# Optimization experiments

Measured on AMD Instinct MI355X. Metric: run time of the kernel, lower is better.

Reference implementation:

```python
import jax, jax.numpy as jnp
import numpy as np

N = 30000       # mesh nodes
E = 150000      # mesh edges
L = 128         # latent_size
STEPS = 5       # message_passing_steps
TW = 5          # time_window
TD = 2          # target_dim
NODE_IN = TD + 1 + 9   # u + load + node_type one-hot = 12
EDGE_IN = 2 + 1 + TD   # rel_mesh + dist + grad_u = 5


def _mlp(x, W1, b1, W2, b2, g, be):
    # Linear -> ReLU -> Linear -> ReLU -> LayerNorm (matches MLP module)
    h = jax.nn.relu(x @ W1 + b1)
    h = jax.nn.relu(h @ W2 + b2)
    mu = jnp.mean(h, axis=-1, keepdims=True)
    var = jnp.mean(jnp.square(h - mu), axis=-1, keepdims=True)
    return g * (h - mu) / jnp.sqrt(var + 1e-5) + be


def setup_inputs() -> dict:
    key = jax.random.key(0)
    ks = iter(jax.random.split(key, 64))
    def nrm(shape, s=0.05):
        return jax.random.normal(next(ks), shape, dtype=jnp.float32) * s
    inp = {}
    inp['mesh_pos'] = jax.random.normal(next(ks), (1, N, 2), dtype=jnp.float32)
    inp['node_type'] = jax.random.normal(next(ks), (1, N, 9), dtype=jnp.float32)
    inp['u'] = jax.random.normal(next(ks), (1, N, TD), dtype=jnp.float32)
    inp['load'] = jax.random.normal(next(ks), (1, N, 1), dtype=jnp.float32)
    inp['senders'] = jax.random.randint(next(ks), (E,), 0, N, dtype=jnp.int32)
    inp['receivers'] = jax.random.randint(next(ks), (E,), 0, N, dtype=jnp.int32)
    # node encoder MLP(12 -> 128)
    inp['enc_node_W1'] = nrm((NODE_IN, L)); inp['enc_node_b1'] = nrm((L,), 0.01)
    inp['enc_node_W2'] = nrm((L, L));       inp['enc_node_b2'] = nrm((L,), 0.01)
    inp['enc_node_g'] = jnp.ones((L,), jnp.float32); inp['enc_node_be'] = jnp.zeros((L,), jnp.float32)
    # edge encoder MLP(5 -> 128)
    inp['enc_edge_W1'] = nrm((EDGE_IN, L)); inp['enc_edge_b1'] = nrm((L,), 0.01)
    inp['enc_edge_W2'] = nrm((L, L));       inp['enc_edge_b2'] = nrm((L,), 0.01)
    inp['enc_edge_g'] = jnp.ones((L,), jnp.float32); inp['enc_edge_be'] = jnp.zeros((L,), jnp.float32)
    # STEPS GraphNetBlocks, params stacked along leading axis for lax.scan
    inp['blk_edge_W1'] = nrm((STEPS, 3 * L, L)); inp['blk_edge_b1'] = nrm((STEPS, L), 0.01)
    inp['blk_edge_W2'] = nrm((STEPS, L, L));     inp['blk_edge_b2'] = nrm((STEPS, L), 0.01)
    inp['blk_edge_g'] = jnp.ones((STEPS, L), jnp.float32); inp['blk_edge_be'] = jnp.zeros((STEPS, L), jnp.float32)
    inp['blk_node_W1'] = nrm((STEPS, 2 * L, L)); inp['blk_node_b1'] = nrm((STEPS, L), 0.01)
    inp['blk_node_W2'] = nrm((STEPS, L, L));     inp['blk_node_b2'] = nrm((STEPS, L), 0.01)
    inp['blk_node_g'] = jnp.ones((STEPS, L), jnp.float32); inp['blk_node_be'] = jnp.zeros((STEPS, L), jnp.float32)
    # decoder: Conv1d(L,8,1) -> Swish -> Conv1d(8, TD*TW, 1); kernel-size-1 conv == per-node linear
    inp['dec_W1'] = nrm((L, 8)); inp['dec_b1'] = nrm((8,), 0.01)
    inp['dec_W2'] = nrm((8, TD * TW)); inp['dec_b2'] = nrm((TD * TW,), 0.01)
    return inp


def reference(mesh_pos, node_type, u, load, senders, receivers,
              enc_node_W1, enc_node_b1, enc_node_W2, enc_node_b2, enc_node_g, enc_node_be,
              enc_edge_W1, enc_edge_b1, enc_edge_W2, enc_edge_b2, enc_edge_g, enc_edge_be,
              blk_edge_W1, blk_edge_b1, blk_edge_W2, blk_edge_b2, blk_edge_g, blk_edge_be,
              blk_node_W1, blk_node_b1, blk_node_W2, blk_node_b2, blk_node_g, blk_node_be,
              dec_W1, dec_b1, dec_W2, dec_b2):
    # --- encode ---
    node_feats = jnp.concatenate([u, load, node_type], axis=-1)        # [1,N,12]
    nl = _mlp(node_feats, enc_node_W1, enc_node_b1, enc_node_W2, enc_node_b2, enc_node_g, enc_node_be)
    rel = mesh_pos[:, senders] - mesh_pos[:, receivers]                # [1,E,2]
    dist = jnp.linalg.norm(rel, axis=-1, keepdims=True)                # [1,E,1]
    grad_u = u[:, senders] - u[:, receivers]                           # [1,E,2]
    ef = jnp.concatenate([rel, dist, grad_u], axis=-1)                 # [1,E,5]
    el = _mlp(ef, enc_edge_W1, enc_edge_b1, enc_edge_W2, enc_edge_b2, enc_edge_g, enc_edge_be)
    n_nodes = nl.shape[1]

    # --- process: GraphNetBlocks with residual connections ---
    def block(carry, p):
        nl, el = carry
        edge_in = jnp.concatenate([nl[:, senders], nl[:, receivers], el], axis=-1)  # [1,E,3L]
        ne = _mlp(edge_in, p['eW1'], p['eb1'], p['eW2'], p['eb2'], p['eg'], p['ebe'])
        aggr = jax.vmap(lambda e: jax.ops.segment_sum(e, receivers, num_segments=n_nodes))(ne)  # [1,N,L]
        node_in = jnp.concatenate([nl, aggr], axis=-1)                 # [1,N,2L]
        nn = _mlp(node_in, p['nW1'], p['nb1'], p['nW2'], p['nb2'], p['ng'], p['nbe'])
        return (nl + nn, el + ne), None

    ps = {'eW1': blk_edge_W1, 'eb1': blk_edge_b1, 'eW2': blk_edge_W2, 'eb2': blk_edge_b2,
          'eg': blk_edge_g, 'ebe': blk_edge_be,
          'nW1': blk_node_W1, 'nb1': blk_node_b1, 'nW2': blk_node_W2, 'nb2': blk_node_b2,
          'ng': blk_node_g, 'nbe': blk_node_be}
    (nl, el), _ = jax.lax.scan(block, (nl, el), ps)

    # --- decode (1x1 Conv1d == per-node linear) ---
    h = nl @ dec_W1 + dec_b1
    h = h * jax.nn.sigmoid(h)                                          # Swish(beta=1)
    decoded = h @ dec_W2 + dec_b2                                      # [1,N,TW*TD]
    dt = jnp.repeat(jnp.arange(1, TW + 1, dtype=decoded.dtype), TD)    # [TW*TD]
    delta = (decoded * dt).reshape(-1, TW, TD).transpose(1, 0, 2)      # [TW,N,TD]
    return delta
```

## Files before the change

### kernel.cpp

```cpp
#include <hip/hip_runtime.h>
#include <hip/hip_bf16.h>

#define LNUM 128
#define NNODES 30000
#define NEDGES 150000
#define NSTEPS 5


typedef _Float16 f16;
typedef __attribute__((ext_vector_type(2))) _Float16 f16x2;
typedef __attribute__((ext_vector_type(8))) _Float16 f16x8;
typedef __attribute__((ext_vector_type(4))) float f32x4;

__device__ __forceinline__ void glds16(const void* g, void* l) {
    __builtin_amdgcn_global_load_lds(
        (const __attribute__((address_space(1))) void*)g,
        (__attribute__((address_space(3))) void*)l, 16, 0, 0);
}

__device__ __forceinline__ void atomic_pk_add(f16* addr, f16 lo, f16 hi) {
#if __has_builtin(__builtin_amdgcn_global_atomic_fadd_v2f16)
    f16x2 v; v[0] = lo; v[1] = hi;
    __builtin_amdgcn_global_atomic_fadd_v2f16(
        (__attribute__((address_space(1))) f16x2*)addr, v);
#else
    uint32_t* p = (uint32_t*)addr;
    uint32_t old = *p, assumed;
    do {
        assumed = old;
        union { uint32_t u; f16 h[2]; } c; c.u = assumed;
        c.h[0] += lo; c.h[1] += hi;
        old = atomicCAS(p, assumed, c.u);
    } while (old != assumed);
#endif
}

template<int ROWS, int K, int KP>
__device__ __forceinline__ void mlp_apply(
    const float* __restrict__ xs, float* __restrict__ hv,
    float* __restrict__ mu_s, float* __restrict__ rs_s,
    const float* __restrict__ W1, const float* __restrict__ b1,
    const float* __restrict__ W2, const float* __restrict__ b2,
    const float* __restrict__ g,  const float* __restrict__ be,
    float out[ROWS])
{
    const int t = threadIdx.x;
    float acc[ROWS];
    {
        const float bb = b1[t];
        #pragma unroll
        for (int r = 0; r < ROWS; r++) acc[r] = bb;
    }
    int k = 0;
    for (; k + 4 <= K; k += 4) {
        const float w0 = W1[(k + 0) * LNUM + t];
        const float w1 = W1[(k + 1) * LNUM + t];
        const float w2 = W1[(k + 2) * LNUM + t];
        const float w3 = W1[(k + 3) * LNUM + t];
        #pragma unroll
        for (int r = 0; r < ROWS; r++) {
            const float4 x = *(const float4*)(xs + r * KP + k);
            acc[r] = fmaf(x.x, w0, acc[r]);
            acc[r] = fmaf(x.y, w1, acc[r]);
            acc[r] = fmaf(x.z, w2, acc[r]);
            acc[r] = fmaf(x.w, w3, acc[r]);
        }
    }
    for (; k < K; ++k) {
        const float w = W1[k * LNUM + t];
        #pragma unroll
        for (int r = 0; r < ROWS; r++) acc[r] = fmaf(xs[r * KP + k], w, acc[r]);
    }
    #pragma unroll
    for (int r = 0; r < ROWS; r++) hv[r * LNUM + t] = fmaxf(acc[r], 0.f);
    __syncthreads();
    {
        const float bb = b2[t];
        #pragma unroll
        for (int r = 0; r < ROWS; r++) acc[r] = bb;
    }
    for (int k2 = 0; k2 < LNUM; k2 += 4) {
        const float w0 = W2[(k2 + 0) * LNUM + t];
        const float w1 = W2[(k2 + 1) * LNUM + t];
        const float w2 = W2[(k2 + 2) * LNUM + t];
        const float w3 = W2[(k2 + 3) * LNUM + t];
        #pragma unroll
        for (int r = 0; r < ROWS; r++) {
            const float4 x = *(const float4*)(hv + r * LNUM + k2);
            acc[r] = fmaf(x.x, w0, acc[r]);
            acc[r] = fmaf(x.y, w1, acc[r]);
            acc[r] = fmaf(x.z, w2, acc[r]);
            acc[r] = fmaf(x.w, w3, acc[r]);
        }
    }
    __syncthreads();
    #pragma unroll
    for (int r = 0; r < ROWS; r++) hv[r * LNUM + t] = fmaxf(acc[r], 0.f);
    __syncthreads();
    if (t < ROWS) {
        float s = 0.f, s2 = 0.f;
        for (int kk = 0; kk < LNUM; kk++) {
            const float v = hv[t * LNUM + kk];
            s += v; s2 += v * v;
        }
        const float m = s * (1.0f / LNUM);
        mu_s[t] = m;
        rs_s[t] = rsqrtf(fmaxf(s2 * (1.0f / LNUM) - m * m, 0.f) + 1e-5f);
    }
    __syncthreads();
    const float gg = g[t], bbe = be[t];
    #pragma unroll
    for (int r = 0; r < ROWS; r++)
        out[r] = fmaf(gg * (hv[r * LNUM + t] - mu_s[r]), rs_s[r], bbe);
}

__global__ __launch_bounds__(128) void encode_nodes_k(
    const float* __restrict__ u, const float* __restrict__ load_,
    const float* __restrict__ ntype,
    const float* __restrict__ W1, const float* __restrict__ b1,
    const float* __restrict__ W2, const float* __restrict__ b2,
    const float* __restrict__ g,  const float* __restrict__ be,
    f16* __restrict__ nl)
{
    constexpr int ROWS = 4, K = 12, KP = 12;
    __shared__ __align__(16) float xs[ROWS * KP];
    __shared__ __align__(16) float hv[ROWS * LNUM];
    __shared__ float mu_s[ROWS], rs_s[ROWS];
    const int t = threadIdx.x;
    const int base = blockIdx.x * ROWS;
    if (t < ROWS * K) {
        const int r = t / K, k = t % K;
        const int n = base + r;
        float v;
        if (k < 2)      v = u[n * 2 + k];
        else if (k < 3) v = load_[n];
        else            v = ntype[n * 9 + (k - 3)];
        xs[r * KP + k] = v;
    }
    __syncthreads();
    float out[ROWS];
    mlp_apply<ROWS, K, KP>(xs, hv, mu_s, rs_s, W1, b1, W2, b2, g, be, out);
    #pragma unroll
    for (int r = 0; r < ROWS; r++) nl[(base + r) * LNUM + t] = (f16)out[r];
}

#define PE1 245760
#define PE2 81920
#define PN1 163840
#define PN2 81920
#define PQ1 4096
#define PQ2 16384
#define PTOT (PE1+PE2+PN1+PN2+PQ1+PQ2)

__global__ __launch_bounds__(256) void prep_w_all_k(
    const float* __restrict__ eW1, const float* __restrict__ eW2,
    const float* __restrict__ nW1, const float* __restrict__ nW2,
    const float* __restrict__ qW1, const float* __restrict__ qW2,
    f16* __restrict__ out)
{
    int j = blockIdx.x * 256 + threadIdx.x;
    if (j >= PTOT) return;
    const float* W; int K, kreal; f16* hi; f16* p = out;
    if (j < PE1) { W = eW1; K = 384; kreal = 384; hi = p; }
    else { p += PE1; j -= PE1;
    if (j < PE2) { W = eW2; K = 128; kreal = 128; hi = p; }
    else { p += PE2; j -= PE2;
    if (j < PN1) { W = nW1; K = 256; kreal = 256; hi = p; }
    else { p += PN1; j -= PN1;
    if (j < PN2) { W = nW2; K = 128; kreal = 128; hi = p; }
    else { p += PN2; j -= PN2;
    if (j < PQ1) { W = qW1; K = 32;  kreal = 5;   hi = p; }
    else { p += PQ1; j -= PQ1;
         { W = qW2; K = 128; kreal = 128; hi = p; } } } } } }
    const int k = j % K;
    const int rem = j / K;
    const int n = rem & 127;
    const int s = rem >> 7;
    const float v = (k < kreal) ? W[((size_t)s * kreal + k) * 128 + n] : 0.f;
    hi[j] = (f16)v;
}

template<int MODE, int NCH1, int K1S>
__global__ __launch_bounds__(256, 5) void mfma_mlp_k(
    const f16* __restrict__ Lat, const float* __restrict__ Fa,
    const float* __restrict__ Fb,
    f16* __restrict__ io, f16* __restrict__ aggr,
    const int* __restrict__ senders, const int* __restrict__ receivers,
    const f16* __restrict__ W1h, const float* __restrict__ b1,
    const f16* __restrict__ W2h, const float* __restrict__ b2,
    const float* __restrict__ gam, const float* __restrict__ bet,
    int nrows)
{
    __shared__ __align__(16) f16 WH[2][4096];
    __shared__ __align__(16) unsigned short Yh[64 * 128];

    const int t  = threadIdx.x;
    const int w  = t >> 6;
    const int l  = t & 63;
    const int lr = l & 15;
    const int lg = l >> 4;
    const int swz = lg ^ ((lr >> 1) & 3);
    const int base = blockIdx.x * 64;

    const int eg  = base + w * 16 + lr;
    const int egc = min(eg, nrows - 1);

    int sv = 0, rv = 0;
    if constexpr (MODE != 1) { sv = senders[egc]; rv = receivers[egc]; }

    float feat[8];
    if constexpr (MODE == 2) {
        const float ax = Fa[sv * 2], ay = Fa[sv * 2 + 1];
        const float bx = Fa[rv * 2], by = Fa[rv * 2 + 1];
        const float rx = ax - bx, ry = ay - by;
        feat[0] = rx; feat[1] = ry; feat[2] = sqrtf(rx * rx + ry * ry);
        feat[3] = Fb[sv * 2] - Fb[rv * 2];
        feat[4] = Fb[sv * 2 + 1] - Fb[rv * 2 + 1];
        feat[5] = 0.f; feat[6] = 0.f; feat[7] = 0.f;
    }

    auto stage = [&](const f16* __restrict__ Wh, const int kst, const int kc,
                     const int buf) {
        #pragma unroll
        for (int i = 0; i < 2; i++) {
            const int c = 2 * w + i;
            const int ophys = c * 1024 + l * 16;
            const int olog  = ophys ^ (((ophys >> 7) & 3) << 4);
            const int row   = olog >> 6;
            const int slot  = (olog >> 4) & 3;
            glds16(Wh + (size_t)row * kst + kc * 32 + slot * 8,
                   (char*)&WH[buf][0] + c * 1024);
        }
    };

    uint4 qnA, qnB, qnC;
    auto prefetchTo = [&](int kc, uint4& q) {
        if constexpr (MODE == 0) {
            const f16* src;
            if (kc < 4)      src = Lat + (size_t)sv  * 128 + kc * 32 + lg * 8;
            else if (kc < 8) src = Lat + (size_t)rv  * 128 + (kc - 4) * 32 + lg * 8;
            else             src = io  + (size_t)egc * 128 + (kc - 8) * 32 + lg * 8;
            q = *(const uint4*)src;
        } else if constexpr (MODE == 1) {
            const f16* src;
            if (kc < 4) src = io  + (size_t)egc * 128 + kc * 32 + lg * 8;
            else        src = Lat + (size_t)egc * 128 + (kc - 4) * 32 + lg * 8;
            q = *(const uint4*)src;
        }
    };

    const f32x4 zero4 = {0.f, 0.f, 0.f, 0.f};
    f32x4 acc[8];
    #pragma unroll
    for (int mf = 0; mf < 8; mf++) acc[mf] = zero4;

    if constexpr (MODE != 2) {
        prefetchTo(0, qnA);
        if constexpr (NCH1 > 1) prefetchTo(1, qnB);
    }
    stage(W1h, K1S, 0, 0);

    #pragma unroll
    for (int kc = 0; kc < NCH1; ++kc) {
        if (MODE != 2 && kc >= 1 && kc + 1 < NCH1)
            asm volatile("s_waitcnt vmcnt(1)" ::: "memory");
        else
            asm volatile("s_waitcnt vmcnt(0)" ::: "memory");
        __builtin_amdgcn_sched_barrier(0);
        __builtin_amdgcn_s_barrier();
        __builtin_amdgcn_sched_barrier(0);
        if (kc + 1 < NCH1) stage(W1h, K1S, kc + 1, (kc + 1) & 1);
        else               stage(W2h, 128,  0,      NCH1 & 1);
        if constexpr (MODE != 2) {
            if (kc + 2 < NCH1) {
                if      ((kc + 2) % 3 == 0) prefetchTo(kc + 2, qnA);
                else if ((kc + 2) % 3 == 1) prefetchTo(kc + 2, qnB);
                else                        prefetchTo(kc + 2, qnC);
            }
        }
        f16x8 XHv, XLv;
        bool useXL = false;
        if constexpr (MODE == 2) {
            union { f16 h[8]; f16x8 v; } uh, ul;
            #pragma unroll
            for (int j = 0; j < 8; j++) {
                const float x = (lg == 0) ? feat[j] : 0.f;
                const f16 h = (f16)x;
                uh.h[j] = h;
                ul.h[j] = (f16)(x - (float)h);
            }
            XHv = uh.v; XLv = ul.v; useXL = true;
        } else {
            union { uint4 q; f16x8 v; } cc;
            cc.q = (kc % 3 == 0) ? qnA : ((kc % 3 == 1) ? qnB : qnC);
            XHv = cc.v;
        }
        #pragma unroll
        for (int mf = 0; mf < 8; mf++) {
            const int off = (mf * 16 + lr) * 64 + (swz << 4);
            const f16x8 wh = *(const f16x8*)((const char*)&WH[kc & 1][0] + off);
            acc[mf] = __builtin_amdgcn_mfma_f32_16x16x32_f16(XHv, wh, acc[mf], 0, 0, 0);
            if (useXL)
                acc[mf] = __builtin_amdgcn_mfma_f32_16x16x32_f16(XLv, wh, acc[mf], 0, 0, 0);
        }
    }

    #pragma unroll
    for (int mf = 0; mf < 8; mf++) {
        const float bb1 = b1[mf * 16 + lr];
        #pragma unroll
        for (int reg = 0; reg < 4; reg++) {
            float v = acc[mf][reg] + bb1;
            v = fmaxf(v, 0.f);
            union { f16 h; unsigned short u; } cc; cc.h = (f16)v;
            const int row = w * 16 + lg * 4 + reg;
            const int cb  = (mf * 16 + lr) * 2;
            *(unsigned short*)((char*)Yh + row * 256 +
                               (cb ^ (((lg * 4 + reg) & 7) << 4))) = cc.u;
        }
        acc[mf] = zero4;
    }

    #pragma unroll
    for (int kc = 0; kc < 4; ++kc) {
        asm volatile("s_waitcnt vmcnt(0)" ::: "memory");
        __builtin_amdgcn_sched_barrier(0);
        __builtin_amdgcn_s_barrier();
        __builtin_amdgcn_sched_barrier(0);
        if (kc + 1 < 4) stage(W2h, 128, kc + 1, (NCH1 + kc + 1) & 1);
        union { uint4 q; f16x8 v; } YH;
        {
            const int row = w * 16 + lr;
            const int cb  = (kc * 32 + lg * 8) * 2;
            YH.q = *(const uint4*)((const char*)Yh + row * 256 +
                                   (cb ^ ((lr & 7) << 4)));
        }
        #pragma unroll
        for (int mf = 0; mf < 8; mf++) {
            const int off = (mf * 16 + lr) * 64 + (swz << 4);
            const f16x8 wh = *(const f16x8*)((const char*)&WH[(NCH1 + kc) & 1][0] + off);
            acc[mf] = __builtin_amdgcn_mfma_f32_16x16x32_f16(YH.v, wh, acc[mf], 0, 0, 0);
        }
    }

    float vv[8][4];
    float s1[4] = {0, 0, 0, 0}, s2[4] = {0, 0, 0, 0};
    #pragma unroll
    for (int mf = 0; mf < 8; mf++) {
        const float bb2 = b2[mf * 16 + lr];
        #pragma unroll
        for (int reg = 0; reg < 4; reg++) {
            float v = acc[mf][reg] + bb2;
            v = fmaxf(v, 0.f);
            vv[mf][reg] = v;
            s1[reg] += v; s2[reg] += v * v;
        }
    }
    #pragma unroll
    for (int m = 1; m < 16; m <<= 1) {
        #pragma unroll
        for (int reg = 0; reg < 4; reg++) {
            s1[reg] += __shfl_xor(s1[reg], m);
            s2[reg] += __shfl_xor(s2[reg], m);
        }
    }
    float gg[8], b8[8];
    #pragma unroll
    for (int mf = 0; mf < 8; mf++) {
        gg[mf] = gam[mf * 16 + lr];
        b8[mf] = bet[mf * 16 + lr];
    }

    #pragma unroll
    for (int reg = 0; reg < 4; reg++) {
        const float mu = s1[reg] * (1.f / 128.f);
        const float rs = rsqrtf(fmaxf(s2[reg] * (1.f / 128.f) - mu * mu, 0.f) + 1e-5f);
        const int row = w * 16 + lg * 4 + reg;
        const int idx = base + row;
        if (idx < nrows) {
            if constexpr (MODE == 0) {
                const int rc = receivers[idx];
                #pragma unroll
                for (int mf = 0; mf < 8; mf++) {
                    const int col = mf * 16 + lr;
                    const float o = gg[mf] * (vv[mf][reg] - mu) * rs + b8[mf];
                    const float op = __shfl_xor(o, 1);
                    if ((lr & 1) == 0)
                        atomic_pk_add(aggr + (size_t)rc * 128 + col,
                                      (f16)o, (f16)op);
                    f16* p = io + (size_t)idx * 128 + col;
                    *p = (f16)((float)*p + o);
                }
            } else if constexpr (MODE == 1) {
                #pragma unroll
                for (int mf = 0; mf < 8; mf++) {
                    const int col = mf * 16 + lr;
                    const float o = gg[mf] * (vv[mf][reg] - mu) * rs + b8[mf];
                    f16* p = io + (size_t)idx * 128 + col;
                    *p = (f16)((float)*p + o);
                }
            } else {
                #pragma unroll
                for (int mf = 0; mf < 8; mf++) {
                    const int col = mf * 16 + lr;
                    const float o = gg[mf] * (vv[mf][reg] - mu) * rs + b8[mf];
                    io[(size_t)idx * 128 + col] = (f16)o;
                }
            }
        }
    }

    if constexpr (MODE == 1) {
        const uint4 z = {0, 0, 0, 0};
        #pragma unroll
        for (int c = 0; c < 4; c++)
            *(uint4*)(aggr + (size_t)egc * 128 + c * 32 + lg * 8) = z;
    }
}

__global__ __launch_bounds__(128) void decode_k(
    const f16* __restrict__ nl,
    const float* __restrict__ W1, const float* __restrict__ b1,
    const float* __restrict__ W2, const float* __restrict__ b2,
    float* __restrict__ out)
{
    constexpr int NPB = 16;
    __shared__ __align__(16) float xs[NPB * LNUM];
    __shared__ float hh[NPB * 8];
    const int t = threadIdx.x;
    const int base = blockIdx.x * NPB;
    for (int r = 0; r < NPB; r++) xs[r * LNUM + t] = (float)nl[(base + r) * LNUM + t];
    __syncthreads();
    {
        const int node = t >> 3, j = t & 7;
        float a = b1[j];
        for (int k = 0; k < LNUM; k++) a = fmaf(xs[node * LNUM + k], W1[k * 8 + j], a);
        hh[node * 8 + j] = a / (1.f + expf(-a));
    }
    __syncthreads();
    for (int idx = t; idx < NPB * 10; idx += 128) {
        const int node = idx / 10, c = idx % 10;
        float a = b2[c];
        #pragma unroll
        for (int j = 0; j < 8; j++) a = fmaf(hh[node * 8 + j], W2[j * 10 + c], a);
        const int tt = c >> 1, d = c & 1;
        out[(size_t)tt * (NNODES * 2) + (size_t)(base + node) * 2 + d] =
            a * (float)(tt + 1);
    }
}

__global__ __launch_bounds__(256) void zero_k(float* __restrict__ p, int n)
{
    const int i = blockIdx.x * 256 + threadIdx.x;
    if (i < n) p[i] = 0.f;
}

extern "C" void kernel_launch(void* const* d_in, const int* in_sizes, int n_in,
                              void* d_out, int out_size, void* d_ws, size_t ws_size,
                              hipStream_t stream) {
    const float* F[34];
    for (int i = 0; i < 34; i++) F[i] = (const float*)d_in[i];
    const int* senders   = (const int*)d_in[4];
    const int* receivers = (const int*)d_in[5];

    const size_t nN = (size_t)NNODES * LNUM;
    const size_t nE = (size_t)NEDGES * LNUM;
    f16* nl16   = (f16*)d_ws;
    f16* el16   = nl16 + nN;
    f16* aggr16 = el16 + nE;
    f16* wb     = aggr16 + nN;
    f16 *eW1h = wb;
    f16 *eW2h = eW1h + PE1;
    f16 *nW1h = eW2h + PE2;
    f16 *nW2h = nW1h + PN1;
    f16 *qW1h = nW2h + PN2;
    f16 *qW2h = qW1h + PQ1;

    prep_w_all_k<<<(PTOT + 255) / 256, 256, 0, stream>>>(
        F[18], F[20], F[24], F[26], F[12], F[14], wb);

    encode_nodes_k<<<NNODES / 4, 128, 0, stream>>>(
        F[2], F[3], F[1], F[6], F[7], F[8], F[9], F[10], F[11], nl16);

    const int egrid = (NEDGES + 63) / 64;
    const int ngrid = (NNODES + 63) / 64;

    mfma_mlp_k<2, 1, 32><<<egrid, 256, 0, stream>>>(
        nullptr, F[0], F[2], el16, nullptr, senders, receivers,
        qW1h, F[13], qW2h, F[15], F[16], F[17], NEDGES);

    zero_k<<<(NNODES * 64 + 255) / 256, 256, 0, stream>>>(
        (float*)aggr16, NNODES * 64);

    for (int s = 0; s < NSTEPS; s++) {
        mfma_mlp_k<0, 12, 384><<<egrid, 256, 0, stream>>>(
            nl16, nullptr, nullptr, el16, aggr16, senders, receivers,
            eW1h + (size_t)s * 384 * 128, F[19] + s * LNUM,
            eW2h + (size_t)s * 128 * 128, F[21] + s * LNUM,
            F[22] + s * LNUM, F[23] + s * LNUM, NEDGES);
        mfma_mlp_k<1, 8, 256><<<ngrid, 256, 0, stream>>>(
            aggr16, nullptr, nullptr, nl16, aggr16, nullptr, nullptr,
            nW1h + (size_t)s * 256 * 128, F[25] + s * LNUM,
            nW2h + (size_t)s * 128 * 128, F[27] + s * LNUM,
            F[28] + s * LNUM, F[29] + s * LNUM, NNODES);
    }

    decode_k<<<NNODES / 16, 128, 0, stream>>>(
        nl16, F[30], F[31], F[32], F[33], (float*)d_out);
}
```

Baseline: 807.6 us.

## Shrink LDS footprint by single-buffering W2 and aliasing Yh with W1 buffer

Merges the weight and hidden-activation shared arrays into one 24 KB buffer. The hidden tile now overlaps the second W1 staging buffer, and the second-layer weights are staged single-buffered, each chunk loaded after the previous chunk's MFMAs behind a barrier. The launch-bounds hint rises from 5 to 6 blocks per CU to allow higher occupancy. The initial prefetch and staging order and the vmcnt wait at the first chunk are also adjusted. The cost is that W2 loads are no longer overlapped with compute, which adds extra barriers in the second GEMM.

```diff
diff --git a/kernel.cpp b/kernel.cpp
--- a/kernel.cpp
+++ b/kernel.cpp
@@ -11,6 +11,8 @@
 typedef __attribute__((ext_vector_type(2))) _Float16 f16x2;
 typedef __attribute__((ext_vector_type(8))) _Float16 f16x8;
 typedef __attribute__((ext_vector_type(4))) float f32x4;
+
+#define SB() __builtin_amdgcn_sched_barrier(0)
 
 __device__ __forceinline__ void glds16(const void* g, void* l) {
     __builtin_amdgcn_global_load_lds(
@@ -181,7 +183,7 @@
 }
 
 template<int MODE, int NCH1, int K1S>
-__global__ __launch_bounds__(256, 5) void mfma_mlp_k(
+__global__ __launch_bounds__(256, 6) void mfma_mlp_k(
     const f16* __restrict__ Lat, const float* __restrict__ Fa,
     const float* __restrict__ Fb,
     f16* __restrict__ io, f16* __restrict__ aggr,
@@ -191,8 +193,7 @@
     const float* __restrict__ gam, const float* __restrict__ bet,
     int nrows)
 {
-    __shared__ __align__(16) f16 WH[2][4096];
-    __shared__ __align__(16) unsigned short Yh[64 * 128];
+    __shared__ __align__(16) char SMEM[24576];
 
     const int t  = threadIdx.x;
     const int w  = t >> 6;
@@ -229,7 +230,7 @@
             const int row   = olog >> 6;
             const int slot  = (olog >> 4) & 3;
             glds16(Wh + (size_t)row * kst + kc * 32 + slot * 8,
-                   (char*)&WH[buf][0] + c * 1024);
+                   SMEM + buf * 8192 + c * 1024);
         }
     };
 
@@ -254,23 +255,24 @@
     #pragma unroll
     for (int mf = 0; mf < 8; mf++) acc[mf] = zero4;
 
-    if constexpr (MODE != 2) {
-        prefetchTo(0, qnA);
-        if constexpr (NCH1 > 1) prefetchTo(1, qnB);
-    }
+    if constexpr (MODE != 2) { prefetchTo(0, qnA); }
+    SB();
     stage(W1h, K1S, 0, 0);
+    SB();
+    if constexpr (MODE != 2) { if constexpr (NCH1 > 1) prefetchTo(1, qnB); }
+    SB();
 
     #pragma unroll
     for (int kc = 0; kc < NCH1; ++kc) {
-        if (MODE != 2 && kc >= 1 && kc + 1 < NCH1)
+        if (MODE != 2 && kc + 1 < NCH1)
             asm volatile("s_waitcnt vmcnt(1)" ::: "memory");
         else
             asm volatile("s_waitcnt vmcnt(0)" ::: "memory");
-        __builtin_amdgcn_sched_barrier(0);
+        SB();
         __builtin_amdgcn_s_barrier();
-        __builtin_amdgcn_sched_barrier(0);
+        SB();
         if (kc + 1 < NCH1) stage(W1h, K1S, kc + 1, (kc + 1) & 1);
-        else               stage(W2h, 128,  0,      NCH1 & 1);
+        SB();
         if constexpr (MODE != 2) {
             if (kc + 2 < NCH1) {
                 if      ((kc + 2) % 3 == 0) prefetchTo(kc + 2, qnA);
@@ -278,6 +280,7 @@
                 else                        prefetchTo(kc + 2, qnC);
             }
         }
+        SB();
         f16x8 XHv, XLv;
         bool useXL = false;
         if constexpr (MODE == 2) {
@@ -298,12 +301,19 @@
         #pragma unroll
         for (int mf = 0; mf < 8; mf++) {
             const int off = (mf * 16 + lr) * 64 + (swz << 4);
-            const f16x8 wh = *(const f16x8*)((const char*)&WH[kc & 1][0] + off);
+            const f16x8 wh = *(const f16x8*)(SMEM + (kc & 1) * 8192 + off);
             acc[mf] = __builtin_amdgcn_mfma_f32_16x16x32_f16(XHv, wh, acc[mf], 0, 0, 0);
             if (useXL)
                 acc[mf] = __builtin_amdgcn_mfma_f32_16x16x32_f16(XLv, wh, acc[mf], 0, 0, 0);
         }
     }
+
+    asm volatile("s_waitcnt lgkmcnt(0)" ::: "memory");
+    SB();
+    __builtin_amdgcn_s_barrier();
+    SB();
+    stage(W2h, 128, 0, 0);
+    SB();
 
     #pragma unroll
     for (int mf = 0; mf < 8; mf++) {
@@ -315,7 +325,7 @@
             union { f16 h; unsigned short u; } cc; cc.h = (f16)v;
             const int row = w * 16 + lg * 4 + reg;
             const int cb  = (mf * 16 + lr) * 2;
-            *(unsigned short*)((char*)Yh + row * 256 +
+            *(unsigned short*)(SMEM + 8192 + row * 256 +
                                (cb ^ (((lg * 4 + reg) & 7) << 4))) = cc.u;
         }
         acc[mf] = zero4;
@@ -324,22 +334,29 @@
     #pragma unroll
     for (int kc = 0; kc < 4; ++kc) {
         asm volatile("s_waitcnt vmcnt(0)" ::: "memory");
-        __builtin_amdgcn_sched_barrier(0);
+        SB();
         __builtin_amdgcn_s_barrier();
-        __builtin_amdgcn_sched_barrier(0);
-        if (kc + 1 < 4) stage(W2h, 128, kc + 1, (NCH1 + kc + 1) & 1);
+        SB();
         union { uint4 q; f16x8 v; } YH;
         {
             const int row = w * 16 + lr;
             const int cb  = (kc * 32 + lg * 8) * 2;
-            YH.q = *(const uint4*)((const char*)Yh + row * 256 +
+            YH.q = *(const uint4*)(SMEM + 8192 + row * 256 +
                                    (cb ^ ((lr & 7) << 4)));
         }
         #pragma unroll
         for (int mf = 0; mf < 8; mf++) {
             const int off = (mf * 16 + lr) * 64 + (swz << 4);
-            const f16x8 wh = *(const f16x8*)((const char*)&WH[(NCH1 + kc) & 1][0] + off);
+            const f16x8 wh = *(const f16x8*)(SMEM + off);
             acc[mf] = __builtin_amdgcn_mfma_f32_16x16x32_f16(YH.v, wh, acc[mf], 0, 0, 0);
+        }
+        if (kc + 1 < 4) {
+            asm volatile("s_waitcnt lgkmcnt(0)" ::: "memory");
+            SB();
+            __builtin_amdgcn_s_barrier();
+            SB();
+            stage(W2h, 128, kc + 1, 0);
+            SB();
         }
     }
 
```

Result: faster. 742.3 us, median of 2 (-8.1%).
